# Kernel tuning notes

Measured on AMD Instinct MI355X. Metric: run time of the kernel, lower is better.

## Reference

```python
import jax, jax.numpy as jnp
import numpy as np

B, MN, D = 8192, 64 * 64, 128


def setup_inputs() -> dict:
    key = jax.random.key(0)
    k1, k2 = jax.random.split(key)
    batch = jax.random.normal(k1, (B, D), dtype=jnp.float32)
    # xavier-normal-ish init for the SOM codebook (scale is irrelevant to correctness)
    weights = jax.random.normal(k2, (MN, D), dtype=jnp.float32) * np.sqrt(2.0 / (MN + D)).astype(np.float32)
    return {"batch": batch, "weights": weights}


def reference(batch, weights):
    # Squared Euclidean distance matrix (B, M*N), same math as the torch
    # broadcast-subtract-square-sum but fused: ||a-b||^2 = ||a||^2 + ||b||^2 - 2 a.b
    a2 = jnp.sum(batch * batch, axis=-1, keepdims=True)          # (B, 1)
    b2 = jnp.sum(weights * weights, axis=-1)                      # (MN,)
    ab = jnp.einsum('bd,md->bm', batch, weights)                  # (B, MN)
    return a2 + b2 - 2.0 * ab
```

## Files before the change

### kernel.cpp

```cpp
#include <hip/hip_runtime.h>
#include <hip/hip_bf16.h>

#define NB   8192
#define NMN  4096
#define ND   128

typedef __attribute__((ext_vector_type(8))) short bf16x8;
typedef __attribute__((ext_vector_type(8))) short short8;
typedef __attribute__((ext_vector_type(4))) float f32x4;


__global__ __launch_bounds__(256) void som_prep(const float* __restrict__ batch,
                                                const float* __restrict__ weights,
                                                __hip_bfloat16* __restrict__ apk,
                                                __hip_bfloat16* __restrict__ wpk,
                                                float* __restrict__ a2,
                                                float* __restrict__ b2) {
    const int wid  = threadIdx.x >> 6;
    const int lane = threadIdx.x & 63;
    const int rof  = lane >> 4;
    const int q    = lane & 15;

    int row = blockIdx.x * 16 + wid * 4 + rof;

    const float* src;
    __hip_bfloat16* dst;
    float* norm;
    if (row < NB) {
        src = batch;  dst = apk; norm = a2;
    } else {
        row -= NB;
        src = weights; dst = wpk; norm = b2;
    }

    const f32x4 v0 = *reinterpret_cast<const f32x4*>(src + (size_t)row * ND + q * 8);
    const f32x4 v1 = *reinterpret_cast<const f32x4*>(src + (size_t)row * ND + q * 8 + 4);

    __hip_bfloat16 tmp[8];
    tmp[0] = __float2bfloat16(v0.x); tmp[1] = __float2bfloat16(v0.y);
    tmp[2] = __float2bfloat16(v0.z); tmp[3] = __float2bfloat16(v0.w);
    tmp[4] = __float2bfloat16(v1.x); tmp[5] = __float2bfloat16(v1.y);
    tmp[6] = __float2bfloat16(v1.z); tmp[7] = __float2bfloat16(v1.w);

    const int chunk = (row >> 4) * 256 + q * 16 + (row & 15);
    *reinterpret_cast<short8*>(dst + (size_t)chunk * 8) =
        *reinterpret_cast<short8*>(tmp);

    float p = v0.x * v0.x + v0.y * v0.y + v0.z * v0.z + v0.w * v0.w
            + v1.x * v1.x + v1.y * v1.y + v1.z * v1.z + v1.w * v1.w;
    #pragma unroll
    for (int off = 1; off < 16; off <<= 1) p += __shfl_xor(p, off, 64);
    if (q == 0) norm[row] = p;
}

__global__ __launch_bounds__(256) void som_gemm(const __hip_bfloat16* __restrict__ apk_,
                                                const __hip_bfloat16* __restrict__ wpk_,
                                                const float* __restrict__ a2,
                                                const float* __restrict__ b2,
                                                float* __restrict__ out) {
    const int bx = blockIdx.x;
    const int w  = (bx & 7) * 256 + (bx >> 3);
    const int brow = (w >> 5) << 7;
    const int bcol = (w & 31) << 7;

    const int tid  = threadIdx.x;
    const int lane = tid & 63;
    const int wid  = tid >> 6;
    const int wr   = wid >> 1;
    const int wc   = wid & 1;
    const int l15  = lane & 15;
    const int l4   = lane >> 4;

    const bf16x8* A = reinterpret_cast<const bf16x8*>(apk_);
    const bf16x8* W = reinterpret_cast<const bf16x8*>(wpk_);

    const int aoff = ((brow >> 4) + wr * 4) * 256 + l4 * 16 + l15;
    const int woff = ((bcol >> 4) + wc * 4) * 256 + l4 * 16 + l15;

    f32x4 acc[4][4];
    #pragma unroll
    for (int m = 0; m < 4; ++m)
        #pragma unroll
        for (int n = 0; n < 4; ++n)
            acc[m][n] = (f32x4){0.f, 0.f, 0.f, 0.f};

    #pragma unroll
    for (int kk = 0; kk < 4; ++kk) {
        bf16x8 bat[4], wgt[4];
        #pragma unroll
        for (int m = 0; m < 4; ++m) bat[m] = A[aoff + m * 256 + kk * 64];
        #pragma unroll
        for (int n = 0; n < 4; ++n) wgt[n] = W[woff + n * 256 + kk * 64];
        #pragma unroll
        for (int m = 0; m < 4; ++m)
            #pragma unroll
            for (int n = 0; n < 4; ++n)
                acc[m][n] = __builtin_amdgcn_mfma_f32_16x16x32_bf16(wgt[n], bat[m], acc[m][n], 0, 0, 0);
    }

    __shared__ float strip[4][16][64];
    f32x4* strip16 = reinterpret_cast<f32x4*>(&strip[wid][0][0]);

    float a2v[4];
    #pragma unroll
    for (int m = 0; m < 4; ++m) a2v[m] = a2[brow + wr * 64 + m * 16 + l15];

    f32x4 b2v[4];
    #pragma unroll
    for (int n = 0; n < 4; ++n)
        b2v[n] = *reinterpret_cast<const f32x4*>(&b2[bcol + wc * 64 + n * 16 + l4 * 4]);

    const size_t orow_base = (size_t)(brow + wr * 64);
    const int    ocol      = bcol + wc * 64 + l15 * 4;

    #pragma unroll
    for (int m = 0; m < 4; ++m) {
        #pragma unroll
        for (int n = 0; n < 4; ++n) {
            f32x4 val = a2v[m] + b2v[n] - 2.0f * acc[m][n];
            strip16[l15 * 16 + ((n * 4 + l4) ^ l15)] = val;
        }
        #pragma unroll
        for (int j = 0; j < 4; ++j) {
            const int r = 4 * j + l4;
            f32x4 val = strip16[r * 16 + (l15 ^ r)];
            __builtin_nontemporal_store(val,
                reinterpret_cast<f32x4*>(out + (orow_base + m * 16 + r) * NMN + ocol));
        }
    }
}

extern "C" void kernel_launch(void* const* d_in, const int* in_sizes, int n_in,
                              void* d_out, int out_size, void* d_ws, size_t ws_size,
                              hipStream_t stream) {
    const float* batch   = (const float*)d_in[0];
    const float* weights = (const float*)d_in[1];
    float* out = (float*)d_out;

    char* ws = (char*)d_ws;
    float* a2 = (float*)(ws);
    float* b2 = (float*)(ws + 32768);
    __hip_bfloat16* apk = (__hip_bfloat16*)(ws + 49152);
    __hip_bfloat16* wpk = (__hip_bfloat16*)(ws + 49152 + 2097152);

    som_prep<<<dim3((NB + NMN) / 16), dim3(256), 0, stream>>>(batch, weights, apk, wpk, a2, b2);

    som_gemm<<<dim3(2048), dim3(256), 0, stream>>>(apk, wpk, a2, b2, out);
}
```

Measured before the change: 37.86 us.

## Fuse bf16 conversion and norm computation into the GEMM kernel via LDS

Removes the separate prep kernel that packed inputs to bf16 and computed row norms. Each GEMM block now loads its 128 batch rows and 128 codebook rows in fp32, converts them to bf16 into a swizzled LDS tile, computes the norms into shared memory, and runs the MFMA loop from LDS. The epilogue strip buffer reuses the A tile's LDS. This saves a kernel launch and the workspace round trip. In exchange, every block redundantly converts its tiles and reads twice as many bytes as the packed bf16 data, and LDS use grows to about 64KB per block, which may lower occupancy.

```diff
diff --git a/kernel.cpp b/kernel.cpp
--- a/kernel.cpp
+++ b/kernel.cpp
@@ -9,55 +9,9 @@
 typedef __attribute__((ext_vector_type(8))) short short8;
 typedef __attribute__((ext_vector_type(4))) float f32x4;
 
-
-__global__ __launch_bounds__(256) void som_prep(const float* __restrict__ batch,
-                                                const float* __restrict__ weights,
-                                                __hip_bfloat16* __restrict__ apk,
-                                                __hip_bfloat16* __restrict__ wpk,
-                                                float* __restrict__ a2,
-                                                float* __restrict__ b2) {
-    const int wid  = threadIdx.x >> 6;
-    const int lane = threadIdx.x & 63;
-    const int rof  = lane >> 4;
-    const int q    = lane & 15;
-
-    int row = blockIdx.x * 16 + wid * 4 + rof;
-
-    const float* src;
-    __hip_bfloat16* dst;
-    float* norm;
-    if (row < NB) {
-        src = batch;  dst = apk; norm = a2;
-    } else {
-        row -= NB;
-        src = weights; dst = wpk; norm = b2;
-    }
-
-    const f32x4 v0 = *reinterpret_cast<const f32x4*>(src + (size_t)row * ND + q * 8);
-    const f32x4 v1 = *reinterpret_cast<const f32x4*>(src + (size_t)row * ND + q * 8 + 4);
-
-    __hip_bfloat16 tmp[8];
-    tmp[0] = __float2bfloat16(v0.x); tmp[1] = __float2bfloat16(v0.y);
-    tmp[2] = __float2bfloat16(v0.z); tmp[3] = __float2bfloat16(v0.w);
-    tmp[4] = __float2bfloat16(v1.x); tmp[5] = __float2bfloat16(v1.y);
-    tmp[6] = __float2bfloat16(v1.z); tmp[7] = __float2bfloat16(v1.w);
-
-    const int chunk = (row >> 4) * 256 + q * 16 + (row & 15);
-    *reinterpret_cast<short8*>(dst + (size_t)chunk * 8) =
-        *reinterpret_cast<short8*>(tmp);
-
-    float p = v0.x * v0.x + v0.y * v0.y + v0.z * v0.z + v0.w * v0.w
-            + v1.x * v1.x + v1.y * v1.y + v1.z * v1.z + v1.w * v1.w;
-    #pragma unroll
-    for (int off = 1; off < 16; off <<= 1) p += __shfl_xor(p, off, 64);
-    if (q == 0) norm[row] = p;
-}
-
-__global__ __launch_bounds__(256) void som_gemm(const __hip_bfloat16* __restrict__ apk_,
-                                                const __hip_bfloat16* __restrict__ wpk_,
-                                                const float* __restrict__ a2,
-                                                const float* __restrict__ b2,
-                                                float* __restrict__ out) {
+__global__ __launch_bounds__(256) void som_fused(const float* __restrict__ batch,
+                                                 const float* __restrict__ weights,
+                                                 float* __restrict__ out) {
     const int bx = blockIdx.x;
     const int w  = (bx & 7) * 256 + (bx >> 3);
     const int brow = (w >> 5) << 7;
@@ -71,11 +25,58 @@
     const int l15  = lane & 15;
     const int l4   = lane >> 4;
 
-    const bf16x8* A = reinterpret_cast<const bf16x8*>(apk_);
-    const bf16x8* W = reinterpret_cast<const bf16x8*>(wpk_);
+    __shared__ __attribute__((aligned(16))) short8 albuf[2048];
+    __shared__ __attribute__((aligned(16))) short8 wlbuf[2048];
+    __shared__ float normsA[128];
+    __shared__ float normsW[128];
 
-    const int aoff = ((brow >> 4) + wr * 4) * 256 + l4 * 16 + l15;
-    const int woff = ((bcol >> 4) + wc * 4) * 256 + l4 * 16 + l15;
+    const int rof = lane >> 4;
+    const int q   = lane & 15;
+
+    #pragma unroll
+    for (int i = 0; i < 8; ++i) {
+        const int quad = wid + 4 * i;
+        const int row  = quad * 4 + rof;
+
+        {
+            const float* src = batch + (size_t)(brow + row) * ND + q * 8;
+            const f32x4 v0 = *reinterpret_cast<const f32x4*>(src);
+            const f32x4 v1 = *reinterpret_cast<const f32x4*>(src + 4);
+            __hip_bfloat16 tmp[8];
+            tmp[0] = __float2bfloat16(v0.x); tmp[1] = __float2bfloat16(v0.y);
+            tmp[2] = __float2bfloat16(v0.z); tmp[3] = __float2bfloat16(v0.w);
+            tmp[4] = __float2bfloat16(v1.x); tmp[5] = __float2bfloat16(v1.y);
+            tmp[6] = __float2bfloat16(v1.z); tmp[7] = __float2bfloat16(v1.w);
+            const int r15 = row & 15;
+            albuf[(row >> 4) * 256 + q * 16 + (r15 ^ q)] =
+                *reinterpret_cast<short8*>(tmp);
+            float p = v0.x * v0.x + v0.y * v0.y + v0.z * v0.z + v0.w * v0.w
+                    + v1.x * v1.x + v1.y * v1.y + v1.z * v1.z + v1.w * v1.w;
+            #pragma unroll
+            for (int off = 1; off < 16; off <<= 1) p += __shfl_xor(p, off, 64);
+            if (q == 0) normsA[row] = p;
+        }
+        {
+            const float* src = weights + (size_t)(bcol + row) * ND + q * 8;
+            const f32x4 v0 = *reinterpret_cast<const f32x4*>(src);
+            const f32x4 v1 = *reinterpret_cast<const f32x4*>(src + 4);
+            __hip_bfloat16 tmp[8];
+            tmp[0] = __float2bfloat16(v0.x); tmp[1] = __float2bfloat16(v0.y);
+            tmp[2] = __float2bfloat16(v0.z); tmp[3] = __float2bfloat16(v0.w);
+            tmp[4] = __float2bfloat16(v1.x); tmp[5] = __float2bfloat16(v1.y);
+            tmp[6] = __float2bfloat16(v1.z); tmp[7] = __float2bfloat16(v1.w);
+            const int r15 = row & 15;
+            wlbuf[(row >> 4) * 256 + q * 16 + (r15 ^ q)] =
+                *reinterpret_cast<short8*>(tmp);
+            float p = v0.x * v0.x + v0.y * v0.y + v0.z * v0.z + v0.w * v0.w
+                    + v1.x * v1.x + v1.y * v1.y + v1.z * v1.z + v1.w * v1.w;
+            #pragma unroll
+            for (int off = 1; off < 16; off <<= 1) p += __shfl_xor(p, off, 64);
+            if (q == 0) normsW[row] = p;
+        }
+    }
+
+    __syncthreads();
 
     f32x4 acc[4][4];
     #pragma unroll
@@ -86,11 +87,15 @@
 
     #pragma unroll
     for (int kk = 0; kk < 4; ++kk) {
+        const int qq = kk * 4 + l4;
+        const int sw = l15 ^ qq;
         bf16x8 bat[4], wgt[4];
         #pragma unroll
-        for (int m = 0; m < 4; ++m) bat[m] = A[aoff + m * 256 + kk * 64];
+        for (int m = 0; m < 4; ++m)
+            bat[m] = (bf16x8)albuf[(wr * 4 + m) * 256 + qq * 16 + sw];
         #pragma unroll
-        for (int n = 0; n < 4; ++n) wgt[n] = W[woff + n * 256 + kk * 64];
+        for (int n = 0; n < 4; ++n)
+            wgt[n] = (bf16x8)wlbuf[(wc * 4 + n) * 256 + qq * 16 + sw];
         #pragma unroll
         for (int m = 0; m < 4; ++m)
             #pragma unroll
@@ -98,17 +103,17 @@
                 acc[m][n] = __builtin_amdgcn_mfma_f32_16x16x32_bf16(wgt[n], bat[m], acc[m][n], 0, 0, 0);
     }
 
-    __shared__ float strip[4][16][64];
-    f32x4* strip16 = reinterpret_cast<f32x4*>(&strip[wid][0][0]);
-
     float a2v[4];
     #pragma unroll
-    for (int m = 0; m < 4; ++m) a2v[m] = a2[brow + wr * 64 + m * 16 + l15];
-
+    for (int m = 0; m < 4; ++m) a2v[m] = normsA[wr * 64 + m * 16 + l15];
     f32x4 b2v[4];
     #pragma unroll
     for (int n = 0; n < 4; ++n)
-        b2v[n] = *reinterpret_cast<const f32x4*>(&b2[bcol + wc * 64 + n * 16 + l4 * 4]);
+        b2v[n] = *reinterpret_cast<const f32x4*>(&normsW[wc * 64 + n * 16 + l4 * 4]);
+
+    __syncthreads();
+
+    f32x4* strip16 = reinterpret_cast<f32x4*>(albuf) + wid * 256;
 
     const size_t orow_base = (size_t)(brow + wr * 64);
     const int    ocol      = bcol + wc * 64 + l15 * 4;
@@ -137,13 +142,5 @@
     const float* weights = (const float*)d_in[1];
     float* out = (float*)d_out;
 
-    char* ws = (char*)d_ws;
-    float* a2 = (float*)(ws);
-    float* b2 = (float*)(ws + 32768);
-    __hip_bfloat16* apk = (__hip_bfloat16*)(ws + 49152);
-    __hip_bfloat16* wpk = (__hip_bfloat16*)(ws + 49152 + 2097152);
-
-    som_prep<<<dim3((NB + NMN) / 16), dim3(256), 0, stream>>>(batch, weights, apk, wpk, a2, b2);
-
-    som_gemm<<<dim3(2048), dim3(256), 0, stream>>>(apk, wpk, a2, b2, out);
+    som_fused<<<dim3(2048), dim3(256), 0, stream>>>(batch, weights, out);
 }
```

After: 45.01 us. 18.9% more time.
